# Performance work log

Hardware: AMD Instinct MI355X
Metric: run time of the kernel (lower is better)

The kernel has to match this reference:

```python
import jax, jax.numpy as jnp
import numpy as np
from jax import lax

T, X, H = 16384, 512, 1024
A_SCALE, A_IDENTITY = 0.1, 0.9


def setup_inputs() -> dict:
    key = jax.random.key(0)
    k1, k2, k3 = jax.random.split(key, 3)
    x_seq = jax.random.normal(k1, (T, X), dtype=jnp.float32)
    h0 = jnp.zeros((H,), dtype=jnp.float32)
    # A_raw is orthogonal-initialized in the module; a random normal matrix
    # is fine as a correctness baseline (orthogonalize for numerical parity).
    A_raw = jax.random.normal(k2, (H, H), dtype=jnp.float32)
    A_raw, _ = jnp.linalg.qr(A_raw)
    B = jax.random.normal(k3, (H, X), dtype=jnp.float32) * (1.0 / np.sqrt(X))  # lecun_normal
    c = jnp.zeros((H,), dtype=jnp.float32)
    return {"x_seq": x_seq, "h0": h0, "A_raw": A_raw, "B": B, "c": c}


def reference(x_seq, h0, A_raw, B, c):
    # A = a_identity * I + a_scale * A_raw
    A = A_IDENTITY * jnp.eye(H, dtype=A_raw.dtype) + A_SCALE * A_raw
    # Precompute input projections for all timesteps in one GEMM: [T, H]
    Bx = x_seq @ B.T + c

    def step(h, bx_t):
        h_new = jnp.tanh(A @ h + bx_t)
        return h_new, h_new

    _, h_all = lax.scan(step, h0, Bx)
    return h_all
```

## Files before the change

kernel.cpp:

```cpp
#include <hip/hip_runtime.h>
#include <math.h>


#define T_STEPS 16384
#define XD 512
#define HD 1024

typedef unsigned int uint32x4 __attribute__((ext_vector_type(4)));

__global__ __launch_bounds__(256) void gemm_bx_kernel(
    const float* __restrict__ x, const float* __restrict__ B,
    const float* __restrict__ c, float* __restrict__ out)
{
    __shared__ __align__(16) float xs[32][68];
    __shared__ __align__(16) float bs[32][68];

    const int tid = threadIdx.x;
    const int t0 = blockIdx.x * 64;
    const int i0 = blockIdx.y * 64;
    const int tx = tid & 15;
    const int ty = tid >> 4;
    const int lr = tid >> 3;
    const int lc = (tid & 7) << 2;

    float acc[4][4] = {{0.f}};

    for (int k0 = 0; k0 < XD; k0 += 32) {
        const float4 xa = *(const float4*)&x[(size_t)(t0 + lr) * XD + k0 + lc];
        const float4 xb = *(const float4*)&x[(size_t)(t0 + lr + 32) * XD + k0 + lc];
        const float4 ba = *(const float4*)&B[(size_t)(i0 + lr) * XD + k0 + lc];
        const float4 bb = *(const float4*)&B[(size_t)(i0 + lr + 32) * XD + k0 + lc];
        __syncthreads();
        xs[lc + 0][lr] = xa.x; xs[lc + 1][lr] = xa.y; xs[lc + 2][lr] = xa.z; xs[lc + 3][lr] = xa.w;
        xs[lc + 0][lr + 32] = xb.x; xs[lc + 1][lr + 32] = xb.y; xs[lc + 2][lr + 32] = xb.z; xs[lc + 3][lr + 32] = xb.w;
        bs[lc + 0][lr] = ba.x; bs[lc + 1][lr] = ba.y; bs[lc + 2][lr] = ba.z; bs[lc + 3][lr] = ba.w;
        bs[lc + 0][lr + 32] = bb.x; bs[lc + 1][lr + 32] = bb.y; bs[lc + 2][lr + 32] = bb.z; bs[lc + 3][lr + 32] = bb.w;
        __syncthreads();
        #pragma unroll
        for (int k = 0; k < 32; ++k) {
            const float4 av = *(const float4*)&xs[k][ty << 2];
            const float4 bv = *(const float4*)&bs[k][tx << 2];
            const float am[4] = {av.x, av.y, av.z, av.w};
            const float bn[4] = {bv.x, bv.y, bv.z, bv.w};
            #pragma unroll
            for (int m = 0; m < 4; ++m)
                #pragma unroll
                for (int n = 0; n < 4; ++n)
                    acc[m][n] = fmaf(am[m], bn[n], acc[m][n]);
        }
    }

    #pragma unroll
    for (int m = 0; m < 4; ++m) {
        const int trow = t0 + (ty << 2) + m;
        #pragma unroll
        for (int n = 0; n < 4; ++n) {
            const int icol = i0 + (tx << 2) + n;
            out[(size_t)trow * HD + icol] = acc[m][n] + c[icol];
        }
    }
}

__global__ void init_slots_kernel(unsigned long long* slots, const float* h0)
{
    const int i = threadIdx.x;
    union { float f; unsigned u; } v; v.f = h0[i];
    slots[3 * HD + i] = (unsigned long long)v.u;
    slots[0 * HD + i] = 0xFFFFFFFF00000000ull;
    slots[1 * HD + i] = 0xFFFFFFFF00000000ull;
    slots[2 * HD + i] = 0xFFFFFFFF00000000ull;
}

__global__ __launch_bounds__(512) void rnn_scan_kernel(
    const float* __restrict__ A_raw, float* out,
    unsigned long long* slots)
{
    const int tid = threadIdx.x;
    const int bid = blockIdx.x;
    const int wave = tid >> 6;
    const int lane = tid & 63;
    const int r0 = (bid << 4) + (wave << 1);

    __shared__ float hlds[2][HD];

    float aw0[16], aw1[16];
    #pragma unroll
    for (int j = 0; j < 16; ++j) {
        const int k = lane + (j << 6);
        float v0 = 0.1f * A_raw[(size_t)r0 * HD + k];
        float v1 = 0.1f * A_raw[(size_t)(r0 + 1) * HD + k];
        if (k == r0) v0 += 0.9f;
        if (k == r0 + 1) v1 += 0.9f;
        aw0[j] = v0; aw1[j] = v1;
    }

    float2 bxn = *(const float2*)&out[r0];

    for (int t = 0; t < T_STEPS; ++t) {
        const float2 bx = bxn;

        const unsigned long long* sp =
            slots + ((size_t)((t + 3) & 3) << 10) + (tid << 1);
        uint32x4 s;
        do {
            asm volatile(
                "global_load_dwordx4 %0, %1, off sc0 sc1\n\t"
                "s_waitcnt vmcnt(0)"
                : "=v"(s) : "v"(sp));
        } while (s.y != (unsigned)t || s.w != (unsigned)t);

        union { unsigned u; float f; } c0, c1; c0.u = s.x; c1.u = s.z;
        *(float2*)&hlds[t & 1][tid << 1] = make_float2(c0.f, c1.f);
        __syncthreads();

        const int tn = (t + 1 < T_STEPS) ? (t + 1) : t;
        bxn = *(const float2*)&out[(size_t)tn * HD + r0];

        const float* hl = hlds[t & 1];
        float p0 = 0.f, p1 = 0.f;
        #pragma unroll
        for (int j = 0; j < 16; ++j) {
            const float hvj = hl[lane + (j << 6)];
            p0 = fmaf(aw0[j], hvj, p0);
            p1 = fmaf(aw1[j], hvj, p1);
        }

        #pragma unroll
        for (int off = 32; off >= 1; off >>= 1) {
            p0 += __shfl_xor(p0, off, 64);
            p1 += __shfl_xor(p1, off, 64);
        }

        if (lane == 0) {
            const float h0n = tanhf(p0 + bx.x);
            const float h1n = tanhf(p1 + bx.y);
            *(float2*)&out[(size_t)t * HD + r0] = make_float2(h0n, h1n);
            union { float f; unsigned u; } u0, u1; u0.f = h0n; u1.f = h1n;
            uint32x4 pkt;
            pkt.x = u0.u; pkt.y = (unsigned)(t + 1);
            pkt.z = u1.u; pkt.w = (unsigned)(t + 1);
            unsigned long long* dp = slots + ((size_t)(t & 3) << 10) + r0;
            asm volatile(
                "global_store_dwordx4 %0, %1, off sc0 sc1"
                :: "v"(dp), "v"(pkt) : "memory");
        }
    }
}

extern "C" void kernel_launch(void* const* d_in, const int* in_sizes, int n_in,
                              void* d_out, int out_size, void* d_ws, size_t ws_size,
                              hipStream_t stream)
{
    const float* x     = (const float*)d_in[0];
    const float* h0    = (const float*)d_in[1];
    const float* A_raw = (const float*)d_in[2];
    const float* B     = (const float*)d_in[3];
    const float* c     = (const float*)d_in[4];
    float* out = (float*)d_out;
    unsigned long long* slots = (unsigned long long*)d_ws;

    dim3 gemm_grid(T_STEPS / 64, HD / 64);
    gemm_bx_kernel<<<gemm_grid, 256, 0, stream>>>(x, B, c, out);
    init_slots_kernel<<<1, HD, 0, stream>>>(slots, h0);
    rnn_scan_kernel<<<64, 512, 0, stream>>>(A_raw, out, slots);
}
```

Before: 24.43 ms.

## Poll full hidden state per wave, drop LDS barrier, four rows per wave

```diff
diff --git a/kernel.cpp b/kernel.cpp
--- a/kernel.cpp
+++ b/kernel.cpp
@@ -7,6 +7,13 @@
 #define HD 1024
 
 typedef unsigned int uint32x4 __attribute__((ext_vector_type(4)));
+
+union fu { float f; unsigned u; };
+
+__device__ __forceinline__ float fast_tanh(float x) {
+    const float e = __expf(2.0f * x);
+    return 1.0f - 2.0f * __builtin_amdgcn_rcpf(e + 1.0f);
+}
 
 __global__ __launch_bounds__(256) void gemm_bx_kernel(
     const float* __restrict__ x, const float* __restrict__ B,
@@ -64,86 +71,111 @@
 __global__ void init_slots_kernel(unsigned long long* slots, const float* h0)
 {
     const int i = threadIdx.x;
-    union { float f; unsigned u; } v; v.f = h0[i];
+    fu v; v.f = h0[i];
     slots[3 * HD + i] = (unsigned long long)v.u;
     slots[0 * HD + i] = 0xFFFFFFFF00000000ull;
     slots[1 * HD + i] = 0xFFFFFFFF00000000ull;
     slots[2 * HD + i] = 0xFFFFFFFF00000000ull;
 }
 
-__global__ __launch_bounds__(512) void rnn_scan_kernel(
-    const float* __restrict__ A_raw, float* out,
+__global__ __launch_bounds__(256) void rnn_scan_kernel(
+    const float* __restrict__ A_raw, float* __restrict__ out,
     unsigned long long* slots)
 {
     const int tid = threadIdx.x;
-    const int bid = blockIdx.x;
     const int wave = tid >> 6;
     const int lane = tid & 63;
-    const int r0 = (bid << 4) + (wave << 1);
+    const int wid = blockIdx.x * 4 + wave;
+    const int r0 = wid << 2;
+    const int sel = lane & 3;
 
-    __shared__ float hlds[2][HD];
-
-    float aw0[16], aw1[16];
+    float2 aw[4][8];
     #pragma unroll
-    for (int j = 0; j < 16; ++j) {
-        const int k = lane + (j << 6);
-        float v0 = 0.1f * A_raw[(size_t)r0 * HD + k];
-        float v1 = 0.1f * A_raw[(size_t)(r0 + 1) * HD + k];
-        if (k == r0) v0 += 0.9f;
-        if (k == r0 + 1) v1 += 0.9f;
-        aw0[j] = v0; aw1[j] = v1;
+    for (int rr = 0; rr < 4; ++rr) {
+        const int r = r0 + rr;
+        #pragma unroll
+        for (int j = 0; j < 8; ++j) {
+            const int k = j * 128 + 2 * lane;
+            float v0 = 0.1f * A_raw[(size_t)r * HD + k];
+            float v1 = 0.1f * A_raw[(size_t)r * HD + k + 1];
+            if (k == r)     v0 += 0.9f;
+            if (k + 1 == r) v1 += 0.9f;
+            aw[rr][j] = make_float2(v0, v1);
+        }
     }
 
-    float2 bxn = *(const float2*)&out[r0];
+    float bx = out[r0 + sel];
 
     for (int t = 0; t < T_STEPS; ++t) {
-        const float2 bx = bxn;
+        const unsigned tagw = (unsigned)t;
+        const char* base0 = (const char*)slots + (((t + 3) & 3) << 13) + (lane << 4);
+        const char* base1 = base0 + 4096;
 
-        const unsigned long long* sp =
-            slots + ((size_t)((t + 3) & 3) << 10) + (tid << 1);
-        uint32x4 s;
+        uint32x4 s0, s1, s2, s3, s4, s5, s6, s7;
+        unsigned bad;
         do {
             asm volatile(
-                "global_load_dwordx4 %0, %1, off sc0 sc1\n\t"
+                "global_load_dwordx4 %0, %[a0], off sc0 sc1\n\t"
+                "global_load_dwordx4 %1, %[a0], off offset:1024 sc0 sc1\n\t"
+                "global_load_dwordx4 %2, %[a0], off offset:2048 sc0 sc1\n\t"
+                "global_load_dwordx4 %3, %[a0], off offset:3072 sc0 sc1\n\t"
+                "global_load_dwordx4 %4, %[a1], off sc0 sc1\n\t"
+                "global_load_dwordx4 %5, %[a1], off offset:1024 sc0 sc1\n\t"
+                "global_load_dwordx4 %6, %[a1], off offset:2048 sc0 sc1\n\t"
+                "global_load_dwordx4 %7, %[a1], off offset:3072 sc0 sc1\n\t"
                 "s_waitcnt vmcnt(0)"
-                : "=v"(s) : "v"(sp));
-        } while (s.y != (unsigned)t || s.w != (unsigned)t);
-
-        union { unsigned u; float f; } c0, c1; c0.u = s.x; c1.u = s.z;
-        *(float2*)&hlds[t & 1][tid << 1] = make_float2(c0.f, c1.f);
-        __syncthreads();
+                : "=v"(s0), "=v"(s1), "=v"(s2), "=v"(s3),
+                  "=v"(s4), "=v"(s5), "=v"(s6), "=v"(s7)
+                : [a0] "v"(base0), [a1] "v"(base1));
+            bad  = (s0.y ^ tagw) | (s0.w ^ tagw);
+            bad |= (s1.y ^ tagw) | (s1.w ^ tagw);
+            bad |= (s2.y ^ tagw) | (s2.w ^ tagw);
+            bad |= (s3.y ^ tagw) | (s3.w ^ tagw);
+            bad |= (s4.y ^ tagw) | (s4.w ^ tagw);
+            bad |= (s5.y ^ tagw) | (s5.w ^ tagw);
+            bad |= (s6.y ^ tagw) | (s6.w ^ tagw);
+            bad |= (s7.y ^ tagw) | (s7.w ^ tagw);
+        } while (__any((int)bad));
 
         const int tn = (t + 1 < T_STEPS) ? (t + 1) : t;
-        bxn = *(const float2*)&out[(size_t)tn * HD + r0];
+        const float bx_next = out[(size_t)tn * HD + r0 + sel];
 
-        const float* hl = hlds[t & 1];
-        float p0 = 0.f, p1 = 0.f;
-        #pragma unroll
-        for (int j = 0; j < 16; ++j) {
-            const float hvj = hl[lane + (j << 6)];
-            p0 = fmaf(aw0[j], hvj, p0);
-            p1 = fmaf(aw1[j], hvj, p1);
-        }
+        float p0 = 0.f, p1 = 0.f, p2 = 0.f, p3 = 0.f;
+        #define ACC(S, J) { fu a_, b_; a_.u = S.x; b_.u = S.z;                 \
+            p0 = fmaf(aw[0][J].x, a_.f, fmaf(aw[0][J].y, b_.f, p0));           \
+            p1 = fmaf(aw[1][J].x, a_.f, fmaf(aw[1][J].y, b_.f, p1));           \
+            p2 = fmaf(aw[2][J].x, a_.f, fmaf(aw[2][J].y, b_.f, p2));           \
+            p3 = fmaf(aw[3][J].x, a_.f, fmaf(aw[3][J].y, b_.f, p3)); }
+        ACC(s0, 0) ACC(s1, 1) ACC(s2, 2) ACC(s3, 3)
+        ACC(s4, 4) ACC(s5, 5) ACC(s6, 6) ACC(s7, 7)
+        #undef ACC
 
         #pragma unroll
         for (int off = 32; off >= 1; off >>= 1) {
             p0 += __shfl_xor(p0, off, 64);
             p1 += __shfl_xor(p1, off, 64);
+            p2 += __shfl_xor(p2, off, 64);
+            p3 += __shfl_xor(p3, off, 64);
         }
 
-        if (lane == 0) {
-            const float h0n = tanhf(p0 + bx.x);
-            const float h1n = tanhf(p1 + bx.y);
-            *(float2*)&out[(size_t)t * HD + r0] = make_float2(h0n, h1n);
-            union { float f; unsigned u; } u0, u1; u0.f = h0n; u1.f = h1n;
+        const float p = (sel == 0) ? p0 : (sel == 1) ? p1 : (sel == 2) ? p2 : p3;
+        const float h = fast_tanh(p + bx);
+
+        if (lane < 4)
+            out[(size_t)t * HD + r0 + lane] = h;
+
+        fu hb; hb.f = h;
+        fu hn; hn.f = __shfl(h, lane ^ 1, 64);
+        if ((lane & ~2) == 0) {
             uint32x4 pkt;
-            pkt.x = u0.u; pkt.y = (unsigned)(t + 1);
-            pkt.z = u1.u; pkt.w = (unsigned)(t + 1);
-            unsigned long long* dp = slots + ((size_t)(t & 3) << 10) + r0;
-            asm volatile(
-                "global_store_dwordx4 %0, %1, off sc0 sc1"
-                :: "v"(dp), "v"(pkt) : "memory");
+            pkt.x = hb.u; pkt.y = (unsigned)(t + 1);
+            pkt.z = hn.u; pkt.w = (unsigned)(t + 1);
+            void* dp = (char*)slots + ((size_t)(t & 3) << 13) + ((size_t)(r0 + lane) << 3);
+            asm volatile("global_store_dwordx4 %0, %1, off sc0 sc1"
+                         :: "v"(dp), "v"(pkt) : "memory");
         }
+
+        bx = bx_next;
     }
 }
 
@@ -162,5 +194,5 @@
     dim3 gemm_grid(T_STEPS / 64, HD / 64);
     gemm_bx_kernel<<<gemm_grid, 256, 0, stream>>>(x, B, c, out);
     init_slots_kernel<<<1, HD, 0, stream>>>(slots, h0);
-    rnn_scan_kernel<<<64, 512, 0, stream>>>(A_raw, out, slots);
+    rnn_scan_kernel<<<64, 256, 0, stream>>>(A_raw, out, slots);
 }
```

New measurement: 32.08 ms. 31.3% more time.
